# Kernel optimization log

Measured on AMD Instinct MI355X. Metric: run time of the kernel, lower is better.

The kernel has to match this reference:

```python
import jax, jax.numpy as jnp
from jax import lax
import numpy as np

B, H, W, C = 4, 128, 128, 128   # C == d_route == n_heads, patch_len == H
OFFSET_RANGE = 5.0              # offset_range_factor == kernel == 5
SCALE = C ** -0.5               # self.scale_factor = d_route**-0.5
CYCLE = 168


def grid_sample_bilinear(img, grid):
    """torch.nn.functional.grid_sample(mode='bilinear', padding_mode='zeros', align_corners=False).
    img: (B,C,H,W); grid: (B,H,W,2) with (x,y) in [-1,1]."""
    Bn, Cn, Hn, Wn = img.shape
    xg = (grid[..., 0] + 1.0) * (Wn / 2.0) - 0.5
    yg = (grid[..., 1] + 1.0) * (Hn / 2.0) - 0.5
    x0 = jnp.floor(xg)
    y0 = jnp.floor(yg)
    img_flat = img.reshape(Bn, Cn, Hn * Wn)
    out = jnp.zeros_like(img)
    for xi in (x0, x0 + 1.0):
        for yi in (y0, y0 + 1.0):
            wgt = (1.0 - jnp.abs(xg - xi)) * (1.0 - jnp.abs(yg - yi))
            valid = (xi >= 0) & (xi <= Wn - 1) & (yi >= 0) & (yi <= Hn - 1)
            ix = jnp.clip(xi, 0, Wn - 1).astype(jnp.int32)
            iy = jnp.clip(yi, 0, Hn - 1).astype(jnp.int32)
            idx = (iy * Wn + ix).reshape(Bn, 1, -1)                      # (B,1,H*W)
            vals = jnp.take_along_axis(img_flat, idx, axis=2).reshape(Bn, Cn, Hn, Wn)
            out = out + vals * (wgt * valid.astype(img.dtype))[:, None, :, :]
    return out


def setup_inputs():
    key = jax.random.key(0)
    ks = jax.random.split(key, 12)
    s = C ** -0.5
    inp = {
        "x": jax.random.normal(ks[0], (B, H, W, C), dtype=jnp.float32),
        "cycle_index": jax.random.randint(ks[1], (B, 128), 0, CYCLE),  # dead path in cycle_mode='None'
        "Wq": jax.random.normal(ks[2], (C, C), dtype=jnp.float32) * s,
        "bq": jnp.zeros((C,), dtype=jnp.float32),
        "Wk": jax.random.normal(ks[3], (C, C), dtype=jnp.float32) * s,
        "bk": jnp.zeros((C,), dtype=jnp.float32),
        "Wv": jax.random.normal(ks[4], (C, C), dtype=jnp.float32) * s,
        "bv": jnp.zeros((C,), dtype=jnp.float32),
        "Wo": jax.random.normal(ks[5], (C, C), dtype=jnp.float32) * s,
        "bo": jnp.zeros((C,), dtype=jnp.float32),
        "Wc1": jax.random.normal(ks[6], (C, C, 5, 5), dtype=jnp.float32) * (1.0 / np.sqrt(C * 25)),
        "bc1": jnp.zeros((C,), dtype=jnp.float32),
        "Wc2": jax.random.normal(ks[7], (2, C), dtype=jnp.float32) * s,   # 1x1 conv, no bias
        "rel_bias": jax.random.normal(ks[8], (1, C, H, 1), dtype=jnp.float32) * 0.02,
    }
    return inp


def reference(x, cycle_index, Wq, bq, Wk, bk, Wv, bv, Wo, bo, Wc1, bc1, Wc2, rel_bias):
    Bn, Hn, Wn, Cn = x.shape
    xc = jnp.transpose(x, (0, 3, 1, 2))                                  # (B,C,H,W)
    # proj_q (1x1 conv) on x (cycle_mode='None')
    q = jnp.einsum('oc,bchw->bohw', Wq, xc) + bq[None, :, None, None]
    # proj_offset: 5x5 conv (pad 2) -> 1x1 conv to 2 channels, tanh * offset_range_factor
    c1 = lax.conv_general_dilated(q, Wc1, (1, 1), ((2, 2), (2, 2)),
                                  dimension_numbers=('NCHW', 'OIHW', 'NCHW')) + bc1[None, :, None, None]
    offset = jnp.tanh(jnp.einsum('oc,bchw->bohw', Wc2, c1)) * OFFSET_RANGE  # (B,2,H,W)
    # create_grid_like + normalize_grid (faithful, incl. x-coord normalized by H and vice versa)
    gx, gy = jnp.meshgrid(jnp.arange(Wn, dtype=x.dtype), jnp.arange(Hn, dtype=x.dtype), indexing='xy')
    grid = jnp.stack([gx, gy], axis=0)                                   # (2,H,W)
    vgrid = grid[None] + offset                                          # (B,2,H,W)
    gh = 2.0 * vgrid[:, 0] / max(Hn - 1, 1) - 1.0
    gw = 2.0 * vgrid[:, 1] / max(Wn - 1, 1) - 1.0
    sgrid = jnp.stack([gh, gw], axis=-1)                                 # (B,H,W,2) = (x,y) for grid_sample
    x_sampled = grid_sample_bilinear(xc, sgrid)                          # (B,C,H,W); n_groups=1 -> rearrange is identity
    k = (jnp.einsum('oc,bchw->bohw', Wk, x_sampled) + bk[None, :, None, None]).reshape(Bn * Cn, Hn, Wn)
    v = (jnp.einsum('oc,bchw->bohw', Wv, x_sampled) + bv[None, :, None, None] + rel_bias).reshape(Bn * Cn, Hn, Wn)
    qr = q.reshape(Bn * Cn, Hn, Wn)
    scores = jnp.einsum('bid,bjd->bij', qr, k) * SCALE                   # (B*C,H,H)
    attn = jax.nn.softmax(scores, axis=-1)
    out = jnp.einsum('bij,bjd->bid', attn, v)                            # (B*C,H,W)
    out = out.reshape(Bn, Hn, Wn, Cn)                                    # faithful raw reshape (as in original)
    return out @ Wo.T + bo
```

## Files before the change

kernel.cpp:

```cpp
#include <hip/hip_runtime.h>
#include <math.h>

#define IMG 16384

typedef short short4v __attribute__((ext_vector_type(4)));
typedef short short8  __attribute__((ext_vector_type(8)));
typedef float floatx4 __attribute__((ext_vector_type(4)));

__device__ __forceinline__ float4 ld4(const float* p) {
    return *reinterpret_cast<const float4*>(p);
}
__device__ __forceinline__ short f2bf(float f) {
    union { float f; unsigned u; } v; v.f = f;
    unsigned r = v.u + 0x7fffu + ((v.u >> 16) & 1u);
    return (short)(r >> 16);
}
__device__ __forceinline__ float bf2f(short s) {
    union { unsigned u; float f; } v;
    v.u = ((unsigned)(unsigned short)s) << 16;
    return v.f;
}

__launch_bounds__(256)
__global__ void k_wprep(const float* __restrict__ Wc1, const float* __restrict__ Wc2,
                        const float* __restrict__ bc1, const float* __restrict__ Wq,
                        const float* __restrict__ bq, const float* __restrict__ Wk,
                        const float* __restrict__ Wv, const float* __restrict__ Wo,
                        float* __restrict__ W2, float* __restrict__ cst,
                        float* __restrict__ b_eff, short* __restrict__ wbf) {
    const int t = threadIdx.x;
    if (blockIdx.x >= 50) {
        int i = (blockIdx.x - 50) * 256 + t;
        int base = i * 8;
        int sel = base >> 14, off = base & 16383;
        const float* s = (sel == 0) ? Wq : (sel == 1) ? Wk : (sel == 2) ? Wv : Wo;
        float4 a = ld4(s + off), b = ld4(s + off + 4);
        short8 o;
        o[0] = f2bf(a.x); o[1] = f2bf(a.y); o[2] = f2bf(a.z); o[3] = f2bf(a.w);
        o[4] = f2bf(b.x); o[5] = f2bf(b.y); o[6] = f2bf(b.z); o[7] = f2bf(b.w);
        *reinterpret_cast<short8*>(wbf + base) = o;
        return;
    }
    __shared__ float U[128];
    __shared__ float red[256];
    __shared__ float wc2[128];
    __shared__ float bql[128];
    const int tt = blockIdx.x;
    const int tch = tt / 25, tap = tt % 25;
    if (t < 128) { wc2[t] = Wc2[tch * 128 + t]; bql[t] = bq[t]; }
    __syncthreads();
    const int c = t & 127, half = t >> 7;
    float p = 0.f;
    for (int o = half * 64; o < half * 64 + 64; ++o)
        p += wc2[o] * Wc1[(o * 128 + c) * 25 + tap];
    red[half * 128 + c] = p;
    __syncthreads();
    if (t < 128) U[t] = red[t] + red[128 + t];
    __syncthreads();
    float p2 = 0.f;
    for (int cc = half * 64; cc < half * 64 + 64; ++cc)
        p2 += U[cc] * Wq[cc * 128 + c];
    red[half * 128 + c] = p2;
    __syncthreads();
    if (t < 128) W2[tt * 128 + t] = red[t] + red[128 + t];
    if (t < 128) red[t] = U[t] * bql[t];
    __syncthreads();
    if (t == 0) {
        float s = 0.f;
        for (int j = 0; j < 128; ++j) s += red[j];
        cst[tt] = s;
    }
    if (tap == 0) {
        __syncthreads();
        if (t < 128) red[t] = wc2[t] * bc1[t];
        __syncthreads();
        if (t == 0) {
            float s = 0.f;
            for (int j = 0; j < 128; ++j) s += red[j];
            b_eff[tch] = s;
        }
    }
}

__launch_bounds__(256)
__global__ void k_off(const float* __restrict__ x, const float* __restrict__ W2,
                      const float* __restrict__ cst, float* __restrict__ P,
                      short* __restrict__ x_bf) {
    __shared__ float Wlds[128 * 68];
    __shared__ float Alds[32 * 68];
    const int t = threadIdx.x;
    const int pg = t & 15, og = t >> 4;
    const int p0 = blockIdx.x * 64;
    const int b = p0 >> 14, pix0 = p0 & (IMG - 1);

    for (int id = t; id < 128 * 64; id += 256) {
        int k = id >> 6, o = id & 63;
        Wlds[k * 68 + o] = (o < 50) ? W2[o * 128 + k] : 0.f;
    }
    float acc[4][4];
#pragma unroll
    for (int i = 0; i < 4; ++i)
#pragma unroll
        for (int j = 0; j < 4; ++j) acc[i][j] = 0.f;

    for (int kc = 0; kc < 128; kc += 32) {
        __syncthreads();
#pragma unroll
        for (int rep = 0; rep < 2; ++rep) {
            int id = rep * 256 + t;
            int m = id >> 3, k4 = (id & 7) * 4;
            float4 v = ld4(x + (size_t)(p0 + m) * 128 + kc + k4);
            Alds[(k4 + 0) * 68 + m] = v.x;
            Alds[(k4 + 1) * 68 + m] = v.y;
            Alds[(k4 + 2) * 68 + m] = v.z;
            Alds[(k4 + 3) * 68 + m] = v.w;
            short4v s = {f2bf(v.x), f2bf(v.y), f2bf(v.z), f2bf(v.w)};
            *reinterpret_cast<short4v*>(x_bf + (size_t)(p0 + m) * 128 + kc + k4) = s;
        }
        __syncthreads();
#pragma unroll
        for (int k = 0; k < 32; ++k) {
            float4 a = *reinterpret_cast<float4*>(&Alds[k * 68 + 4 * pg]);
            float4 wv = *reinterpret_cast<float4*>(&Wlds[(kc + k) * 68 + 4 * og]);
            float av[4] = {a.x, a.y, a.z, a.w};
            float wf[4] = {wv.x, wv.y, wv.z, wv.w};
#pragma unroll
            for (int i = 0; i < 4; ++i)
#pragma unroll
                for (int j = 0; j < 4; ++j)
                    acc[i][j] = fmaf(av[i], wf[j], acc[i][j]);
        }
    }
    __syncthreads();
#pragma unroll
    for (int j = 0; j < 4; ++j) {
        int o = 4 * og + j;
        float c = (o < 50) ? cst[o] : 0.f;
        *reinterpret_cast<float4*>(&Wlds[o * 68 + 4 * pg]) =
            make_float4(acc[0][j] + c, acc[1][j] + c, acc[2][j] + c, acc[3][j] + c);
    }
    __syncthreads();
    for (int id = t; id < 50 * 16; id += 256) {
        int o = id >> 4, px4 = (id & 15) * 4;
        float4 v = *reinterpret_cast<float4*>(&Wlds[o * 68 + px4]);
        *reinterpret_cast<float4*>(P + ((size_t)(b * 50 + o)) * IMG + pix0 + px4) = v;
    }
}

__launch_bounds__(256, 2)
__global__ void k_fused3(const float* __restrict__ P, const float* __restrict__ b_eff,
                         const short* __restrict__ x_bf, const short* __restrict__ wbf,
                         const float* __restrict__ bq, const float* __restrict__ bk,
                         const float* __restrict__ bv, const float* __restrict__ rel,
                         short* __restrict__ q_bf, short* __restrict__ k_bf,
                         short* __restrict__ v_bf) {
    __shared__ __align__(16) char smem[70656];
    float* rowsP  = (float*)smem;
    short* stg    = (short*)smem;
    short* xsT    = (short*)(smem + 34816);
    float* offs_l = (float*)(smem + 69632);

    const int t = threadIdx.x;
    const int w = t >> 6, l = t & 63, l15 = l & 15, quad = l >> 4;
    const int mh = w >> 1, nh = w & 1;
    const int bh = blockIdx.x;
    const int b = bh >> 7, h = bh & 127;

    for (int id = t; id < 1600; id += 256) {
        int o = id >> 5, q4 = (id & 31) * 4;
        int di = (o % 25) / 5;
        int r = h + di - 2;
        float4 v = make_float4(0.f, 0.f, 0.f, 0.f);
        if (r >= 0 && r < 128)
            v = ld4(P + ((size_t)(b * 50 + o)) * IMG + r * 128 + q4);
        *reinterpret_cast<float4*>(&rowsP[o * 132 + q4]) = v;
    }
    __syncthreads();
    {
        int wp = t & 127, tc = t >> 7;
        float acc = 0.f;
#pragma unroll
        for (int di = 0; di < 5; ++di)
#pragma unroll
            for (int dj = 0; dj < 5; ++dj) {
                int wj = wp + dj - 2;
                if (wj >= 0 && wj < 128)
                    acc += rowsP[(tc * 25 + di * 5 + dj) * 132 + wj];
            }
        offs_l[tc * 128 + wp] = tanhf(acc + b_eff[tc]) * 5.0f;
    }
    __syncthreads();

    for (int id = t; id < 2048; id += 256) {
        int px = id >> 4, c8 = id & 15;
        float ox = offs_l[px];
        float oy = offs_l[128 + px];
        float xg = ((float)px + ox) * (128.0f / 127.0f) - 0.5f;
        float yg = ((float)h  + oy) * (128.0f / 127.0f) - 0.5f;
        float x0f = floorf(xg), y0f = floorf(yg);
        float fx = xg - x0f, fy = yg - y0f;
        int x0 = (int)x0f, y0 = (int)y0f;
        float s[8];
#pragma unroll
        for (int r = 0; r < 8; ++r) s[r] = 0.f;
#pragma unroll
        for (int tap = 0; tap < 4; ++tap) {
            int xi = x0 + (tap & 1), yi = y0 + (tap >> 1);
            float wgt = ((tap & 1) ? fx : 1.f - fx) * ((tap >> 1) ? fy : 1.f - fy);
            if (xi >= 0 && xi < 128 && yi >= 0 && yi < 128) {
                short8 v = *reinterpret_cast<const short8*>(
                    x_bf + (((size_t)(b * 128 + yi)) * 128 + xi) * 128 + c8 * 8);
#pragma unroll
                for (int r = 0; r < 8; ++r) s[r] = fmaf(wgt, bf2f(v[r]), s[r]);
            }
        }
        short8 o;
#pragma unroll
        for (int r = 0; r < 8; ++r) o[r] = f2bf(s[r]);
        *reinterpret_cast<short8*>(&xsT[px * 136 + c8 * 8]) = o;
    }

    {
        const short* xr = x_bf + ((size_t)(b * 128 + h)) * 128 * 128;
        floatx4 acc[4][4];
#pragma unroll
        for (int im = 0; im < 4; ++im)
#pragma unroll
            for (int in = 0; in < 4; ++in)
                acc[im][in] = (floatx4){0.f, 0.f, 0.f, 0.f};
#pragma unroll
        for (int kc = 0; kc < 128; kc += 32) {
            short8 af[4], bf_[4];
#pragma unroll
            for (int im = 0; im < 4; ++im)
                af[im] = *reinterpret_cast<const short8*>(
                    xr + (mh * 64 + im * 16 + l15) * 128 + kc + quad * 8);
#pragma unroll
            for (int in = 0; in < 4; ++in)
                bf_[in] = *reinterpret_cast<const short8*>(
                    wbf + (nh * 64 + in * 16 + l15) * 128 + kc + quad * 8);
#pragma unroll
            for (int im = 0; im < 4; ++im)
#pragma unroll
                for (int in = 0; in < 4; ++in)
                    acc[im][in] = __builtin_amdgcn_mfma_f32_16x16x32_bf16(
                        af[im], bf_[in], acc[im][in], 0, 0, 0);
        }
        __syncthreads();
#pragma unroll
        for (int in = 0; in < 4; ++in) {
            int o = nh * 64 + in * 16 + l15;
            float bb = bq[o];
#pragma unroll
            for (int im = 0; im < 4; ++im) {
                int row0 = mh * 64 + im * 16 + quad * 4;
                short4v s = {f2bf(acc[im][in][0] + bb), f2bf(acc[im][in][1] + bb),
                             f2bf(acc[im][in][2] + bb), f2bf(acc[im][in][3] + bb)};
                *reinterpret_cast<short4v*>(&stg[o * 136 + row0]) = s;
            }
        }
    }
    __syncthreads();
    for (int id = t; id < 2048; id += 256) {
        int o = id >> 4, seg = id & 15;
        *reinterpret_cast<short8*>(
            q_bf + ((size_t)(b * 128 + o)) * IMG + h * 128 + seg * 8)
            = *reinterpret_cast<const short8*>(&stg[o * 136 + seg * 8]);
    }

    {
        floatx4 ak[4][4], av[4][4];
#pragma unroll
        for (int im = 0; im < 4; ++im)
#pragma unroll
            for (int in = 0; in < 4; ++in) {
                ak[im][in] = (floatx4){0.f, 0.f, 0.f, 0.f};
                av[im][in] = (floatx4){0.f, 0.f, 0.f, 0.f};
            }
#pragma unroll
        for (int kc = 0; kc < 128; kc += 32) {
            short8 af[4], bk_[4], bv_[4];
#pragma unroll
            for (int im = 0; im < 4; ++im)
                af[im] = *reinterpret_cast<const short8*>(
                    &xsT[(mh * 64 + im * 16 + l15) * 136 + kc + quad * 8]);
#pragma unroll
            for (int in = 0; in < 4; ++in) {
                bk_[in] = *reinterpret_cast<const short8*>(
                    wbf + 16384 + (nh * 64 + in * 16 + l15) * 128 + kc + quad * 8);
                bv_[in] = *reinterpret_cast<const short8*>(
                    wbf + 32768 + (nh * 64 + in * 16 + l15) * 128 + kc + quad * 8);
            }
#pragma unroll
            for (int im = 0; im < 4; ++im)
#pragma unroll
                for (int in = 0; in < 4; ++in) {
                    ak[im][in] = __builtin_amdgcn_mfma_f32_16x16x32_bf16(
                        af[im], bk_[in], ak[im][in], 0, 0, 0);
                    av[im][in] = __builtin_amdgcn_mfma_f32_16x16x32_bf16(
                        af[im], bv_[in], av[im][in], 0, 0, 0);
                }
        }
        __syncthreads();
#pragma unroll
        for (int in = 0; in < 4; ++in) {
            int o = nh * 64 + in * 16 + l15;
            float bbk = bk[o];
            float bbv = bv[o] + rel[o * 128 + h];
#pragma unroll
            for (int im = 0; im < 4; ++im) {
                int row0 = mh * 64 + im * 16 + quad * 4;
                short4v sk = {f2bf(ak[im][in][0] + bbk), f2bf(ak[im][in][1] + bbk),
                              f2bf(ak[im][in][2] + bbk), f2bf(ak[im][in][3] + bbk)};
                short4v sv = {f2bf(av[im][in][0] + bbv), f2bf(av[im][in][1] + bbv),
                              f2bf(av[im][in][2] + bbv), f2bf(av[im][in][3] + bbv)};
                *reinterpret_cast<short4v*>(&stg[o * 136 + row0]) = sk;
                *reinterpret_cast<short4v*>(&xsT[o * 136 + row0]) = sv;
            }
        }
    }
    __syncthreads();
    for (int id = t; id < 4096; id += 256) {
        int sel = id >> 11;
        int o = (id >> 4) & 127, seg = id & 15;
        short* dst = sel ? v_bf : k_bf;
        const short* src = sel ? xsT : stg;
        *reinterpret_cast<short8*>(
            dst + ((size_t)(b * 128 + o)) * IMG + h * 128 + seg * 8)
            = *reinterpret_cast<const short8*>(&src[o * 136 + seg * 8]);
    }
}

__launch_bounds__(256, 2)
__global__ void k_attn3(const short* __restrict__ q_bf, const short* __restrict__ k_bf,
                        const short* __restrict__ v_bf, const short* __restrict__ WoB,
                        const float* __restrict__ bo, float* __restrict__ outp) {
    __shared__ __align__(16) short Pb[128 * 136];
    __shared__ __align__(16) short vT[128 * 136];
    __shared__ float redm[2 * 128];
    __shared__ float reds[2 * 128];

    const int t = threadIdx.x;
    const int w = t >> 6, l = t & 63, l15 = l & 15, quad = l >> 4;
    const int mh = w >> 1, nh = w & 1;
    const size_t hb = (size_t)blockIdx.x * IMG;
    const short* qp = q_bf + hb;
    const short* kp = k_bf + hb;
    const short* vp = v_bf + hb;

    for (int id = t; id < 2048; id += 256) {
        int j = id >> 4, seg = id & 15;
        short8 v8 = *reinterpret_cast<const short8*>(vp + j * 128 + seg * 8);
        int cbase = ((j >> 3) ^ seg) & 15;
        int off = j & 7;
#pragma unroll
        for (int r = 0; r < 8; ++r)
            vT[(seg * 8 + r) * 136 + cbase * 8 + off] = v8[r];
    }

    floatx4 acc[4][4];
#pragma unroll
    for (int im = 0; im < 4; ++im)
#pragma unroll
        for (int in = 0; in < 4; ++in)
            acc[im][in] = (floatx4){0.f, 0.f, 0.f, 0.f};

#pragma unroll
    for (int kc = 0; kc < 128; kc += 32) {
        short8 af[4], bf_[4];
#pragma unroll
        for (int im = 0; im < 4; ++im)
            af[im] = *reinterpret_cast<const short8*>(
                qp + (mh * 64 + im * 16 + l15) * 128 + kc + quad * 8);
#pragma unroll
        for (int in = 0; in < 4; ++in)
            bf_[in] = *reinterpret_cast<const short8*>(
                kp + (nh * 64 + in * 16 + l15) * 128 + kc + quad * 8);
#pragma unroll
        for (int im = 0; im < 4; ++im)
#pragma unroll
            for (int in = 0; in < 4; ++in)
                acc[im][in] = __builtin_amdgcn_mfma_f32_16x16x32_bf16(
                    af[im], bf_[in], acc[im][in], 0, 0, 0);
    }

    const float scale = 0.08838834764831845f;
    float mloc[4][4];
#pragma unroll
    for (int im = 0; im < 4; ++im)
#pragma unroll
        for (int r = 0; r < 4; ++r) {
            float m = acc[im][0][r];
#pragma unroll
            for (int in = 1; in < 4; ++in) m = fmaxf(m, acc[im][in][r]);
            mloc[im][r] = m;
        }
#pragma unroll
    for (int mask = 1; mask < 16; mask <<= 1)
#pragma unroll
        for (int im = 0; im < 4; ++im)
#pragma unroll
            for (int r = 0; r < 4; ++r)
                mloc[im][r] = fmaxf(mloc[im][r], __shfl_xor(mloc[im][r], mask, 64));
    if (l15 == 0) {
#pragma unroll
        for (int im = 0; im < 4; ++im)
#pragma unroll
            for (int r = 0; r < 4; ++r)
                redm[nh * 128 + mh * 64 + im * 16 + quad * 4 + r] = mloc[im][r];
    }
    __syncthreads();
    float sloc[4][4];
#pragma unroll
    for (int im = 0; im < 4; ++im)
#pragma unroll
        for (int r = 0; r < 4; ++r) {
            int row = mh * 64 + im * 16 + quad * 4 + r;
            float m = fmaxf(redm[row], redm[128 + row]);
            float ss = 0.f;
#pragma unroll
            for (int in = 0; in < 4; ++in) {
                float e = __expf((acc[im][in][r] - m) * scale);
                acc[im][in][r] = e;
                ss += e;
            }
            sloc[im][r] = ss;
        }
#pragma unroll
    for (int mask = 1; mask < 16; mask <<= 1)
#pragma unroll
        for (int im = 0; im < 4; ++im)
#pragma unroll
            for (int r = 0; r < 4; ++r)
                sloc[im][r] += __shfl_xor(sloc[im][r], mask, 64);
    if (l15 == 0) {
#pragma unroll
        for (int im = 0; im < 4; ++im)
#pragma unroll
            for (int r = 0; r < 4; ++r)
                reds[nh * 128 + mh * 64 + im * 16 + quad * 4 + r] = sloc[im][r];
    }
    __syncthreads();
#pragma unroll
    for (int im = 0; im < 4; ++im)
#pragma unroll
        for (int r = 0; r < 4; ++r) {
            int row = mh * 64 + im * 16 + quad * 4 + r;
            float inv = 1.0f / (reds[row] + reds[128 + row]);
#pragma unroll
            for (int in = 0; in < 4; ++in) {
                int col = nh * 64 + in * 16 + l15;
                Pb[row * 136 + col] = f2bf(acc[im][in][r] * inv);
            }
        }
    __syncthreads();

#pragma unroll
    for (int im = 0; im < 4; ++im)
#pragma unroll
        for (int in = 0; in < 4; ++in)
            acc[im][in] = (floatx4){0.f, 0.f, 0.f, 0.f};
#pragma unroll
    for (int kc = 0; kc < 128; kc += 32) {
        short8 af[4], bf_[4];
#pragma unroll
        for (int im = 0; im < 4; ++im)
            af[im] = *reinterpret_cast<const short8*>(
                &Pb[(mh * 64 + im * 16 + l15) * 136 + kc + quad * 8]);
#pragma unroll
        for (int in = 0; in < 4; ++in) {
            int dRow = nh * 64 + in * 16 + l15;
            int cphys = (((kc >> 3) + quad) ^ (dRow >> 3)) & 15;
            bf_[in] = *reinterpret_cast<const short8*>(
                &vT[dRow * 136 + cphys * 8]);
        }
#pragma unroll
        for (int im = 0; im < 4; ++im)
#pragma unroll
            for (int in = 0; in < 4; ++in)
                acc[im][in] = __builtin_amdgcn_mfma_f32_16x16x32_bf16(
                    af[im], bf_[in], acc[im][in], 0, 0, 0);
    }
    __syncthreads();
#pragma unroll
    for (int im = 0; im < 4; ++im)
#pragma unroll
        for (int in = 0; in < 4; ++in) {
            int col = nh * 64 + in * 16 + l15;
#pragma unroll
            for (int r = 0; r < 4; ++r) {
                int row = mh * 64 + im * 16 + quad * 4 + r;
                Pb[row * 136 + col] = f2bf(acc[im][in][r]);
            }
        }
    __syncthreads();

    float bb[4];
#pragma unroll
    for (int in = 0; in < 4; ++in) bb[in] = bo[nh * 64 + in * 16 + l15];
#pragma unroll
    for (int im = 0; im < 4; ++im)
#pragma unroll
        for (int in = 0; in < 4; ++in)
            acc[im][in] = (floatx4){0.f, 0.f, 0.f, 0.f};
#pragma unroll
    for (int kc = 0; kc < 128; kc += 32) {
        short8 af[4], bf_[4];
#pragma unroll
        for (int im = 0; im < 4; ++im)
            af[im] = *reinterpret_cast<const short8*>(
                &Pb[(mh * 64 + im * 16 + l15) * 136 + kc + quad * 8]);
#pragma unroll
        for (int in = 0; in < 4; ++in)
            bf_[in] = *reinterpret_cast<const short8*>(
                WoB + (nh * 64 + in * 16 + l15) * 128 + kc + quad * 8);
#pragma unroll
        for (int im = 0; im < 4; ++im)
#pragma unroll
            for (int in = 0; in < 4; ++in)
                acc[im][in] = __builtin_amdgcn_mfma_f32_16x16x32_bf16(
                    af[im], bf_[in], acc[im][in], 0, 0, 0);
    }
#pragma unroll
    for (int im = 0; im < 4; ++im)
#pragma unroll
        for (int in = 0; in < 4; ++in) {
            int col = nh * 64 + in * 16 + l15;
#pragma unroll
            for (int r = 0; r < 4; ++r) {
                int row = mh * 64 + im * 16 + quad * 4 + r;
                outp[hb + (size_t)row * 128 + col] = acc[im][in][r] + bb[in];
            }
        }
}

extern "C" void kernel_launch(void* const* d_in, const int* in_sizes, int n_in,
                              void* d_out, int out_size, void* d_ws, size_t ws_size,
                              hipStream_t stream) {
    const float* x   = (const float*)d_in[0];
    const float* Wq  = (const float*)d_in[2];
    const float* bq  = (const float*)d_in[3];
    const float* Wk  = (const float*)d_in[4];
    const float* bk  = (const float*)d_in[5];
    const float* Wv  = (const float*)d_in[6];
    const float* bv  = (const float*)d_in[7];
    const float* Wo  = (const float*)d_in[8];
    const float* bo  = (const float*)d_in[9];
    const float* Wc1 = (const float*)d_in[10];
    const float* bc1 = (const float*)d_in[11];
    const float* Wc2 = (const float*)d_in[12];
    const float* rel = (const float*)d_in[13];

    char* wsb = (char*)d_ws;
    short* q_bf  = (short*)(wsb);
    short* k_bf  = (short*)(wsb + 1ull * 16777216);
    short* v_bf  = (short*)(wsb + 2ull * 16777216);
    short* x_bf  = (short*)(wsb + 3ull * 16777216);
    float* P     = (float*)(wsb + 4ull * 16777216);
    float* W2    = (float*)(wsb + 4ull * 16777216 + 13107200);
    float* cst   = W2 + 6400;
    float* b_eff = cst + 64;
    short* wbf   = (short*)(b_eff + 16);
    float* outp  = (float*)d_out;

    hipLaunchKernelGGL(k_wprep,  dim3(82),   dim3(256), 0, stream, Wc1, Wc2, bc1, Wq, bq,
                       Wk, Wv, Wo, W2, cst, b_eff, wbf);
    hipLaunchKernelGGL(k_off,    dim3(1024), dim3(256), 0, stream, x, W2, cst, P, x_bf);
    hipLaunchKernelGGL(k_fused3, dim3(512),  dim3(256), 0, stream, P, b_eff, x_bf, wbf,
                       bq, bk, bv, rel, q_bf, k_bf, v_bf);
    hipLaunchKernelGGL(k_attn3,  dim3(512),  dim3(256), 0, stream, q_bf, k_bf, v_bf,
                       wbf + 49152, bo, outp);
}
```

Measured before the change: 223.7 us.

## Move offset projection GEMM to bf16 MFMA with split hi/lo precision

Replaces the FP32 scalar-FMA GEMM in k_off, which projects x onto the 50 offset-conv weights, with MFMA 16x16x32 bf16 instructions. Both operands are split into high and low bf16 parts and three MFMA products are summed to keep close to FP32 accuracy. k_wprep now also emits the split bf16 weights, padded to 64 rows. Each block covers 128 pixels with fragments loaded straight from global memory rather than through an LDS transpose, trading three times the MFMA work and some precision for fewer FP32 ALU cycles.

```diff
diff --git a/kernel.cpp b/kernel.cpp
--- a/kernel.cpp
+++ b/kernel.cpp
@@ -27,9 +27,16 @@
                         const float* __restrict__ bq, const float* __restrict__ Wk,
                         const float* __restrict__ Wv, const float* __restrict__ Wo,
                         float* __restrict__ W2, float* __restrict__ cst,
-                        float* __restrict__ b_eff, short* __restrict__ wbf) {
+                        float* __restrict__ b_eff, short* __restrict__ wbf,
+                        short* __restrict__ w2h, short* __restrict__ w2l) {
     const int t = threadIdx.x;
     if (blockIdx.x >= 50) {
+        if (blockIdx.x == 50) {
+            for (int i = t; i < 14 * 128; i += 256) {
+                w2h[6400 + i] = 0;
+                w2l[6400 + i] = 0;
+            }
+        }
         int i = (blockIdx.x - 50) * 256 + t;
         int base = i * 8;
         int sel = base >> 14, off = base & 16383;
@@ -62,7 +69,13 @@
         p2 += U[cc] * Wq[cc * 128 + c];
     red[half * 128 + c] = p2;
     __syncthreads();
-    if (t < 128) W2[tt * 128 + t] = red[t] + red[128 + t];
+    if (t < 128) {
+        float vv = red[t] + red[128 + t];
+        W2[tt * 128 + t] = vv;
+        short hh = f2bf(vv);
+        w2h[tt * 128 + t] = hh;
+        w2l[tt * 128 + t] = f2bf(vv - bf2f(hh));
+    }
     if (t < 128) red[t] = U[t] * bql[t];
     __syncthreads();
     if (t == 0) {
@@ -82,67 +95,79 @@
     }
 }
 
-__launch_bounds__(256)
-__global__ void k_off(const float* __restrict__ x, const float* __restrict__ W2,
-                      const float* __restrict__ cst, float* __restrict__ P,
-                      short* __restrict__ x_bf) {
-    __shared__ float Wlds[128 * 68];
-    __shared__ float Alds[32 * 68];
+__launch_bounds__(256, 2)
+__global__ void k_off(const float* __restrict__ x, const short* __restrict__ w2h,
+                      const short* __restrict__ w2l, const float* __restrict__ cst,
+                      float* __restrict__ P, short* __restrict__ x_bf) {
+    __shared__ __align__(16) float stage[64 * 132];
     const int t = threadIdx.x;
-    const int pg = t & 15, og = t >> 4;
-    const int p0 = blockIdx.x * 64;
+    const int w = t >> 6, l = t & 63, l15 = l & 15, quad = l >> 4;
+    const int p0 = blockIdx.x * 128;
     const int b = p0 >> 14, pix0 = p0 & (IMG - 1);
 
-    for (int id = t; id < 128 * 64; id += 256) {
-        int k = id >> 6, o = id & 63;
-        Wlds[k * 68 + o] = (o < 50) ? W2[o * 128 + k] : 0.f;
-    }
-    float acc[4][4];
-#pragma unroll
-    for (int i = 0; i < 4; ++i)
-#pragma unroll
-        for (int j = 0; j < 4; ++j) acc[i][j] = 0.f;
-
+    floatx4 acc[2][4];
+#pragma unroll
+    for (int im = 0; im < 2; ++im)
+#pragma unroll
+        for (int in = 0; in < 4; ++in) acc[im][in] = (floatx4){0.f, 0.f, 0.f, 0.f};
+
+    const float* xb = x + (size_t)p0 * 128;
+    short* xbb = x_bf + (size_t)p0 * 128;
+
+#pragma unroll
     for (int kc = 0; kc < 128; kc += 32) {
-        __syncthreads();
-#pragma unroll
-        for (int rep = 0; rep < 2; ++rep) {
-            int id = rep * 256 + t;
-            int m = id >> 3, k4 = (id & 7) * 4;
-            float4 v = ld4(x + (size_t)(p0 + m) * 128 + kc + k4);
-            Alds[(k4 + 0) * 68 + m] = v.x;
-            Alds[(k4 + 1) * 68 + m] = v.y;
-            Alds[(k4 + 2) * 68 + m] = v.z;
-            Alds[(k4 + 3) * 68 + m] = v.w;
-            short4v s = {f2bf(v.x), f2bf(v.y), f2bf(v.z), f2bf(v.w)};
-            *reinterpret_cast<short4v*>(x_bf + (size_t)(p0 + m) * 128 + kc + k4) = s;
-        }
-        __syncthreads();
-#pragma unroll
-        for (int k = 0; k < 32; ++k) {
-            float4 a = *reinterpret_cast<float4*>(&Alds[k * 68 + 4 * pg]);
-            float4 wv = *reinterpret_cast<float4*>(&Wlds[(kc + k) * 68 + 4 * og]);
-            float av[4] = {a.x, a.y, a.z, a.w};
-            float wf[4] = {wv.x, wv.y, wv.z, wv.w};
-#pragma unroll
-            for (int i = 0; i < 4; ++i)
-#pragma unroll
-                for (int j = 0; j < 4; ++j)
-                    acc[i][j] = fmaf(av[i], wf[j], acc[i][j]);
-        }
-    }
-    __syncthreads();
-#pragma unroll
-    for (int j = 0; j < 4; ++j) {
-        int o = 4 * og + j;
-        float c = (o < 50) ? cst[o] : 0.f;
-        *reinterpret_cast<float4*>(&Wlds[o * 68 + 4 * pg]) =
-            make_float4(acc[0][j] + c, acc[1][j] + c, acc[2][j] + c, acc[3][j] + c);
-    }
-    __syncthreads();
-    for (int id = t; id < 50 * 16; id += 256) {
-        int o = id >> 4, px4 = (id & 15) * 4;
-        float4 v = *reinterpret_cast<float4*>(&Wlds[o * 68 + px4]);
+        short8 ah[2], al[2];
+#pragma unroll
+        for (int im = 0; im < 2; ++im) {
+            int row = w * 32 + im * 16 + l15;
+            const float* src = xb + row * 128 + kc + quad * 8;
+            float4 f0 = ld4(src), f1 = ld4(src + 4);
+            float fv[8] = {f0.x, f0.y, f0.z, f0.w, f1.x, f1.y, f1.z, f1.w};
+            short8 h8, l8;
+#pragma unroll
+            for (int r = 0; r < 8; ++r) {
+                short hh = f2bf(fv[r]);
+                h8[r] = hh;
+                l8[r] = f2bf(fv[r] - bf2f(hh));
+            }
+            ah[im] = h8; al[im] = l8;
+            *reinterpret_cast<short8*>(xbb + row * 128 + kc + quad * 8) = h8;
+        }
+        short8 bh[4], bl[4];
+#pragma unroll
+        for (int in = 0; in < 4; ++in) {
+            int o = in * 16 + l15;
+            bh[in] = *reinterpret_cast<const short8*>(w2h + o * 128 + kc + quad * 8);
+            bl[in] = *reinterpret_cast<const short8*>(w2l + o * 128 + kc + quad * 8);
+        }
+#pragma unroll
+        for (int im = 0; im < 2; ++im)
+#pragma unroll
+            for (int in = 0; in < 4; ++in) {
+                acc[im][in] = __builtin_amdgcn_mfma_f32_16x16x32_bf16(
+                    ah[im], bh[in], acc[im][in], 0, 0, 0);
+                acc[im][in] = __builtin_amdgcn_mfma_f32_16x16x32_bf16(
+                    ah[im], bl[in], acc[im][in], 0, 0, 0);
+                acc[im][in] = __builtin_amdgcn_mfma_f32_16x16x32_bf16(
+                    al[im], bh[in], acc[im][in], 0, 0, 0);
+            }
+    }
+#pragma unroll
+    for (int im = 0; im < 2; ++im)
+#pragma unroll
+        for (int in = 0; in < 4; ++in) {
+            int o = in * 16 + l15;
+            int row0 = w * 32 + im * 16 + quad * 4;
+            *reinterpret_cast<float4*>(&stage[o * 132 + row0]) =
+                make_float4(acc[im][in][0], acc[im][in][1],
+                            acc[im][in][2], acc[im][in][3]);
+        }
+    __syncthreads();
+    for (int id = t; id < 50 * 32; id += 256) {
+        int o = id >> 5, px4 = (id & 31) * 4;
+        float c = cst[o];
+        float4 v = *reinterpret_cast<float4*>(&stage[o * 132 + px4]);
+        v.x += c; v.y += c; v.z += c; v.w += c;
         *reinterpret_cast<float4*>(P + ((size_t)(b * 50 + o)) * IMG + pix0 + px4) = v;
     }
 }
@@ -561,11 +586,13 @@
     float* cst   = W2 + 6400;
     float* b_eff = cst + 64;
     short* wbf   = (short*)(b_eff + 16);
+    short* w2h   = wbf + 65536;
+    short* w2l   = w2h + 8192;
     float* outp  = (float*)d_out;
 
     hipLaunchKernelGGL(k_wprep,  dim3(82),   dim3(256), 0, stream, Wc1, Wc2, bc1, Wq, bq,
-                       Wk, Wv, Wo, W2, cst, b_eff, wbf);
-    hipLaunchKernelGGL(k_off,    dim3(1024), dim3(256), 0, stream, x, W2, cst, P, x_bf);
+                       Wk, Wv, Wo, W2, cst, b_eff, wbf, w2h, w2l);
+    hipLaunchKernelGGL(k_off,    dim3(512),  dim3(256), 0, stream, x, w2h, w2l, cst, P, x_bf);
     hipLaunchKernelGGL(k_fused3, dim3(512),  dim3(256), 0, stream, P, b_eff, x_bf, wbf,
                        bq, bk, bv, rel, q_bf, k_bf, v_bf);
     hipLaunchKernelGGL(k_attn3,  dim3(512),  dim3(256), 0, stream, q_bf, k_bf, v_bf,
```

New measurement: 204.9 us. 8.4% less time.
